# Kernel tuning notes

Measured on AMD Instinct MI355X. Metric: run time of the kernel, lower is better.

## Reference

```python
import jax, jax.numpy as jnp
import numpy as np

N_USERS = 100000
EMBED_DIM = 128
N_EDGES = 640000


def setup_inputs() -> dict:
    key = jax.random.key(0)
    k1, k2, k3, k4, k5, k6 = jax.random.split(key, 6)
    # Xavier-normal-ish scale for embedding table
    emb = jax.random.normal(k1, (N_USERS, EMBED_DIM), dtype=jnp.float32) * 0.02
    s = 1.0 / np.sqrt(EMBED_DIM)
    W_l = jax.random.normal(k2, (EMBED_DIM, EMBED_DIM), dtype=jnp.float32) * s
    b_l = jax.random.normal(k3, (EMBED_DIM,), dtype=jnp.float32) * 0.01
    W_r = jax.random.normal(k4, (EMBED_DIM, EMBED_DIM), dtype=jnp.float32) * s
    src = jax.random.randint(k5, (N_EDGES,), 0, N_USERS, dtype=jnp.int64)
    dst = jax.random.randint(k6, (N_EDGES,), 0, N_USERS, dtype=jnp.int64)
    return {"emb": emb, "W_l": W_l, "b_l": b_l, "W_r": W_r, "src": src, "dst": dst}


def reference(emb, W_l, b_l, W_r, src, dst):
    # GraphSAGE (mean aggr) over the full user embedding table.
    # messages gathered from source nodes: [E, D]
    msgs = emb[src]
    agg = jax.ops.segment_sum(msgs, dst, num_segments=N_USERS)  # [N, D]
    deg = jax.ops.segment_sum(jnp.ones((dst.shape[0],), dtype=emb.dtype), dst,
                              num_segments=N_USERS)
    agg = agg / jnp.maximum(deg, 1.0)[:, None]  # mean over neighbors
    # out = lin_l(mean neighbors) + lin_r(self); bias on lin_l only (PyG SAGEConv)
    out = agg @ W_l.T + b_l + emb @ W_r.T
    # dropout (p=0) and batchnorm (is_norm=False) are identity here
    return out
```

## Files before the change

### kernel.cpp

```cpp
#include <hip/hip_runtime.h>
#include <hip/hip_bf16.h>

#define N_USERS   100000
#define EMBED_DIM 128
#define N_EDGES   640000
#define ZERO_ROW  N_USERS

typedef __bf16 bf16x8 __attribute__((ext_vector_type(8)));
typedef float  f32x4  __attribute__((ext_vector_type(4)));

#define OFF_COUNTS 25600256
#define OFF_TOTAL  26000256
#define OFF_START  26000384
#define OFF_CURSOR 26400384
#define OFF_PERM   26800384
#define OFF_WLSW   30560384
#define OFF_WRSW   30593152
#define OFF_AGGB   30625920

__device__ __forceinline__ unsigned short f2bf_rne(float f) {
    union { float f; unsigned u; } c; c.f = f;
    unsigned u = c.u + 0x7fffu + ((c.u >> 16) & 1u);
    return (unsigned short)(u >> 16);
}
__device__ __forceinline__ float bf2f_lo(unsigned u) {
    union { float f; unsigned u; } c; c.u = u << 16;
    return c.f;
}
__device__ __forceinline__ float bf2f_hi(unsigned u) {
    union { float f; unsigned u; } c; c.u = u & 0xffff0000u;
    return c.f;
}

__global__ __launch_bounds__(256) void k_init(const float* __restrict__ emb,
                                              const float* __restrict__ Wl,
                                              const float* __restrict__ Wr,
                                              const int* __restrict__ dst,
                                              unsigned short* __restrict__ embb,
                                              int* __restrict__ counts,
                                              unsigned short* __restrict__ wlsw,
                                              unsigned short* __restrict__ wrsw) {
    int i = blockIdx.x * 256 + threadIdx.x;
    if (i < 2048) {
        int li = i & 63;
        int kt = (i >> 6) & 3;
        int jt = i >> 8;
        int row  = jt * 16 + (li & 15);
        int colb = kt * 32 + ((li >> 4) << 3);
        const float4* pl = (const float4*)(Wl + row * 128 + colb);
        const float4* pr = (const float4*)(Wr + row * 128 + colb);
        float4 l0 = pl[0], l1 = pl[1];
        float4 r0 = pr[0], r1 = pr[1];
        int o = i * 8;
        wlsw[o+0] = f2bf_rne(l0.x); wlsw[o+1] = f2bf_rne(l0.y);
        wlsw[o+2] = f2bf_rne(l0.z); wlsw[o+3] = f2bf_rne(l0.w);
        wlsw[o+4] = f2bf_rne(l1.x); wlsw[o+5] = f2bf_rne(l1.y);
        wlsw[o+6] = f2bf_rne(l1.z); wlsw[o+7] = f2bf_rne(l1.w);
        wrsw[o+0] = f2bf_rne(r0.x); wrsw[o+1] = f2bf_rne(r0.y);
        wrsw[o+2] = f2bf_rne(r0.z); wrsw[o+3] = f2bf_rne(r0.w);
        wrsw[o+4] = f2bf_rne(r1.x); wrsw[o+5] = f2bf_rne(r1.y);
        wrsw[o+6] = f2bf_rne(r1.z); wrsw[o+7] = f2bf_rne(r1.w);
    }
    if (i < 16) {
        int4 z = {0, 0, 0, 0};
        ((int4*)(embb + (size_t)ZERO_ROW * EMBED_DIM))[i] = z;
    }
    float4 a = ((const float4*)emb)[i * 2 + 0];
    float4 b = ((const float4*)emb)[i * 2 + 1];
    int4 p;
    p.x = (int)f2bf_rne(a.x) | ((int)f2bf_rne(a.y) << 16);
    p.y = (int)f2bf_rne(a.z) | ((int)f2bf_rne(a.w) << 16);
    p.z = (int)f2bf_rne(b.x) | ((int)f2bf_rne(b.y) << 16);
    p.w = (int)f2bf_rne(b.z) | ((int)f2bf_rne(b.w) << 16);
    ((int4*)embb)[i] = p;
    if (i < N_EDGES) atomicAdd(&counts[dst[i]], 1);
}

__global__ __launch_bounds__(256) void k_alloc(const int* __restrict__ counts,
                                               int* __restrict__ start,
                                               int* __restrict__ cursor,
                                               int* __restrict__ total,
                                               int* __restrict__ perm) {
    int i    = blockIdx.x * 256 + threadIdx.x;
    int lane = threadIdx.x & 63;
    int wv   = threadIdx.x >> 6;
    int4 c4 = {0, 0, 0, 0};
    if (i < 25000) c4 = ((const int4*)counts)[i];
    int4 p4;
    p4.x = (c4.x + 3) & ~3;
    p4.y = (c4.y + 3) & ~3;
    p4.z = (c4.z + 3) & ~3;
    p4.w = (c4.w + 3) & ~3;
    int csum = p4.x + p4.y + p4.z + p4.w;
    int pre = csum;
#pragma unroll
    for (int d = 1; d < 64; d <<= 1) {
        int v = __shfl_up(pre, d);
        if (lane >= d) pre += v;
    }
    __shared__ int swv[4];
    __shared__ int sgbase;
    if (lane == 63) swv[wv] = pre;
    __syncthreads();
    if (threadIdx.x == 0)
        sgbase = atomicAdd(total, swv[0] + swv[1] + swv[2] + swv[3]);
    __syncthreads();
    int waveoff = 0;
    for (int w = 0; w < wv; w++) waveoff += swv[w];
    int base = sgbase + waveoff + (pre - csum);
    if (i < 25000) {
        int4 s;
        s.x = base;
        s.y = s.x + p4.x;
        s.z = s.y + p4.y;
        s.w = s.z + p4.z;
        ((int4*)start)[i]  = s;
        ((int4*)cursor)[i] = s;
        for (int k = c4.x; k < p4.x; k++) perm[s.x + k] = ZERO_ROW;
        for (int k = c4.y; k < p4.y; k++) perm[s.y + k] = ZERO_ROW;
        for (int k = c4.z; k < p4.z; k++) perm[s.z + k] = ZERO_ROW;
        for (int k = c4.w; k < p4.w; k++) perm[s.w + k] = ZERO_ROW;
    }
}

__global__ __launch_bounds__(256) void k_perm(const int* __restrict__ src,
                                              const int* __restrict__ dst,
                                              int* __restrict__ cursor,
                                              int* __restrict__ perm) {
    int e = blockIdx.x * 256 + threadIdx.x;
    if (e < N_EDGES) {
        int pos = atomicAdd(&cursor[dst[e]], 1);
        perm[pos] = src[e];
    }
}

__global__ __launch_bounds__(256) void k_aggregate(const unsigned short* __restrict__ embb,
                                                   const int* __restrict__ start,
                                                   const int* __restrict__ counts,
                                                   const int* __restrict__ perm,
                                                   unsigned short* __restrict__ aggb) {
    int gw   = (blockIdx.x * 256 + threadIdx.x) >> 6;
    int lane = threadIdx.x & 63;
    int nA = gw * 2;
    int nB = nA + 1;
    int sA = start[nA], cntA = counts[nA];
    int sB = start[nB], cntB = counts[nB];
    int ga = (cntA + 3) >> 2;
    int gb = (cntB + 3) >> 2;
    int gmin = ga < gb ? ga : gb;
    float2 accA = {0.f, 0.f}, accB = {0.f, 0.f};
    const unsigned short* ep = embb;
    int off = lane * 2;

    int t = 0;
    for (; t < gmin; t++) {
        int4 ia = ((const int4*)(perm + sA))[t];
        int4 ib = ((const int4*)(perm + sB))[t];
        unsigned a0 = *(const unsigned*)(ep + (size_t)ia.x * EMBED_DIM + off);
        unsigned a1 = *(const unsigned*)(ep + (size_t)ia.y * EMBED_DIM + off);
        unsigned a2 = *(const unsigned*)(ep + (size_t)ia.z * EMBED_DIM + off);
        unsigned a3 = *(const unsigned*)(ep + (size_t)ia.w * EMBED_DIM + off);
        unsigned b0 = *(const unsigned*)(ep + (size_t)ib.x * EMBED_DIM + off);
        unsigned b1 = *(const unsigned*)(ep + (size_t)ib.y * EMBED_DIM + off);
        unsigned b2 = *(const unsigned*)(ep + (size_t)ib.z * EMBED_DIM + off);
        unsigned b3 = *(const unsigned*)(ep + (size_t)ib.w * EMBED_DIM + off);
        accA.x += (bf2f_lo(a0) + bf2f_lo(a1)) + (bf2f_lo(a2) + bf2f_lo(a3));
        accA.y += (bf2f_hi(a0) + bf2f_hi(a1)) + (bf2f_hi(a2) + bf2f_hi(a3));
        accB.x += (bf2f_lo(b0) + bf2f_lo(b1)) + (bf2f_lo(b2) + bf2f_lo(b3));
        accB.y += (bf2f_hi(b0) + bf2f_hi(b1)) + (bf2f_hi(b2) + bf2f_hi(b3));
    }
    for (int ta = t; ta < ga; ta++) {
        int4 ia = ((const int4*)(perm + sA))[ta];
        unsigned a0 = *(const unsigned*)(ep + (size_t)ia.x * EMBED_DIM + off);
        unsigned a1 = *(const unsigned*)(ep + (size_t)ia.y * EMBED_DIM + off);
        unsigned a2 = *(const unsigned*)(ep + (size_t)ia.z * EMBED_DIM + off);
        unsigned a3 = *(const unsigned*)(ep + (size_t)ia.w * EMBED_DIM + off);
        accA.x += (bf2f_lo(a0) + bf2f_lo(a1)) + (bf2f_lo(a2) + bf2f_lo(a3));
        accA.y += (bf2f_hi(a0) + bf2f_hi(a1)) + (bf2f_hi(a2) + bf2f_hi(a3));
    }
    for (int tb = t; tb < gb; tb++) {
        int4 ib = ((const int4*)(perm + sB))[tb];
        unsigned b0 = *(const unsigned*)(ep + (size_t)ib.x * EMBED_DIM + off);
        unsigned b1 = *(const unsigned*)(ep + (size_t)ib.y * EMBED_DIM + off);
        unsigned b2 = *(const unsigned*)(ep + (size_t)ib.z * EMBED_DIM + off);
        unsigned b3 = *(const unsigned*)(ep + (size_t)ib.w * EMBED_DIM + off);
        accB.x += (bf2f_lo(b0) + bf2f_lo(b1)) + (bf2f_lo(b2) + bf2f_lo(b3));
        accB.y += (bf2f_hi(b0) + bf2f_hi(b1)) + (bf2f_hi(b2) + bf2f_hi(b3));
    }
    float invA = (cntA > 0) ? 1.0f / (float)cntA : 0.0f;
    float invB = (cntB > 0) ? 1.0f / (float)cntB : 0.0f;
    unsigned oA = (unsigned)f2bf_rne(accA.x * invA) | ((unsigned)f2bf_rne(accA.y * invA) << 16);
    unsigned oB = (unsigned)f2bf_rne(accB.x * invB) | ((unsigned)f2bf_rne(accB.y * invB) << 16);
    *(unsigned*)(aggb + (size_t)nA * EMBED_DIM + off) = oA;
    *(unsigned*)(aggb + (size_t)nB * EMBED_DIM + off) = oB;
}

#define LDS_S 136
__global__ __launch_bounds__(256) void k_matmul(const unsigned short* __restrict__ aggb,
                                                const unsigned short* __restrict__ wlsw,
                                                const unsigned short* __restrict__ wrsw,
                                                const unsigned short* __restrict__ embb,
                                                const float* __restrict__ bl,
                                                float* __restrict__ out) {
    __shared__ unsigned short sa[32 * LDS_S];
    __shared__ unsigned short se[32 * LDS_S];
    int tid  = threadIdx.x;
    int wave = tid >> 6;
    int lane = tid & 63;
    int quad = lane >> 4;
    int m    = lane & 15;
    int jt0  = wave * 2;
    int node0 = blockIdx.x * 32;

    bf16x8 wl[2][4], wr[2][4];
#pragma unroll
    for (int jj = 0; jj < 2; jj++) {
#pragma unroll
        for (int kt = 0; kt < 4; kt++) {
            size_t o = (size_t)((((jt0 + jj) * 4 + kt) * 64 + lane)) * 8;
            wl[jj][kt] = *(const bf16x8*)((const __bf16*)wlsw + o);
            wr[jj][kt] = *(const bf16x8*)((const __bf16*)wrsw + o);
        }
    }
    float bias[2];
    bias[0] = bl[(jt0 + 0) * 16 + m];
    bias[1] = bl[(jt0 + 1) * 16 + m];

    const int4* aslab = (const int4*)(aggb + (size_t)node0 * EMBED_DIM);
    const int4* eslab = (const int4*)(embb + (size_t)node0 * EMBED_DIM);
#pragma unroll
    for (int p = 0; p < 2; p++) {
        int g   = p * 256 + tid;
        int row = g >> 4;
        int c   = g & 15;
        int4 va = aslab[g];
        int4 ve = eslab[g];
        *(int4*)(sa + row * LDS_S + c * 8) = va;
        *(int4*)(se + row * LDS_S + c * 8) = ve;
    }
    __syncthreads();

    bf16x8 af[2][4], ef[2][4];
#pragma unroll
    for (int rt = 0; rt < 2; rt++) {
#pragma unroll
        for (int kt = 0; kt < 4; kt++) {
            int o = (rt * 16 + m) * LDS_S + kt * 32 + quad * 8;
            af[rt][kt] = *(const bf16x8*)(sa + o);
            ef[rt][kt] = *(const bf16x8*)(se + o);
        }
    }

#pragma unroll
    for (int rt = 0; rt < 2; rt++) {
        f32x4 acc[2] = {{0.f,0.f,0.f,0.f}, {0.f,0.f,0.f,0.f}};
#pragma unroll
        for (int kt = 0; kt < 4; kt++) {
#pragma unroll
            for (int jj = 0; jj < 2; jj++) {
                acc[jj] = __builtin_amdgcn_mfma_f32_16x16x32_bf16(af[rt][kt], wl[jj][kt], acc[jj], 0, 0, 0);
                acc[jj] = __builtin_amdgcn_mfma_f32_16x16x32_bf16(ef[rt][kt], wr[jj][kt], acc[jj], 0, 0, 0);
            }
        }
#pragma unroll
        for (int jj = 0; jj < 2; jj++) {
#pragma unroll
            for (int r = 0; r < 4; r++) {
                int orow = node0 + rt * 16 + quad * 4 + r;
                out[(size_t)orow * EMBED_DIM + (jt0 + jj) * 16 + m] = acc[jj][r] + bias[jj];
            }
        }
    }
}

extern "C" void kernel_launch(void* const* d_in, const int* in_sizes, int n_in,
                              void* d_out, int out_size, void* d_ws, size_t ws_size,
                              hipStream_t stream) {
    const float* emb = (const float*)d_in[0];
    const float* Wl  = (const float*)d_in[1];
    const float* bl  = (const float*)d_in[2];
    const float* Wr  = (const float*)d_in[3];
    const int*   src = (const int*)d_in[4];
    const int*   dst = (const int*)d_in[5];
    float* out = (float*)d_out;

    char* ws = (char*)d_ws;
    unsigned short* embb   = (unsigned short*)ws;
    int*            counts = (int*)(ws + OFF_COUNTS);
    int*            total  = (int*)(ws + OFF_TOTAL);
    int*            start  = (int*)(ws + OFF_START);
    int*            cursor = (int*)(ws + OFF_CURSOR);
    int*            perm   = (int*)(ws + OFF_PERM);
    unsigned short* wlsw   = (unsigned short*)(ws + OFF_WLSW);
    unsigned short* wrsw   = (unsigned short*)(ws + OFF_WRSW);
    unsigned short* aggb   = (unsigned short*)(ws + OFF_AGGB);

    hipMemsetAsync(ws + OFF_COUNTS, 0, (OFF_TOTAL - OFF_COUNTS) + 4, stream);

    k_init<<<6250, 256, 0, stream>>>(emb, Wl, Wr, dst, embb, counts, wlsw, wrsw);
    k_alloc<<<98, 256, 0, stream>>>(counts, start, cursor, total, perm);
    k_perm<<<2500, 256, 0, stream>>>(src, dst, cursor, perm);
    k_aggregate<<<12500, 256, 0, stream>>>(embb, start, counts, perm, aggb);
    k_matmul<<<3125, 256, 0, stream>>>(aggb, wlsw, wrsw, embb, bl, out);
}
```

Before: 214.2 us.

## Fuse neighbor aggregation into the MFMA matmul kernel via shared memory

Merges the separate aggregation and matmul kernels into one kernel. Each block gathers and averages neighbor rows for its 32 nodes and writes the bf16 means straight into LDS instead of a global agg buffer. This removes a kernel launch and the write and re-read of the 25 MB aggregate, and it prefetches the self-embedding slab ahead of the gather. The cost is fewer, heavier blocks: each wave now handles 8 nodes serially, which may expose gather latency. A launch-bounds hint of 4 blocks per CU and a smaller fragment register footprint are added to keep occupancy up.

```diff
diff --git a/kernel.cpp b/kernel.cpp
--- a/kernel.cpp
+++ b/kernel.cpp
@@ -16,7 +16,6 @@
 #define OFF_PERM   26800384
 #define OFF_WLSW   30560384
 #define OFF_WRSW   30593152
-#define OFF_AGGB   30625920
 
 __device__ __forceinline__ unsigned short f2bf_rne(float f) {
     union { float f; unsigned u; } c; c.f = f;
@@ -134,74 +133,15 @@
     }
 }
 
-__global__ __launch_bounds__(256) void k_aggregate(const unsigned short* __restrict__ embb,
-                                                   const int* __restrict__ start,
-                                                   const int* __restrict__ counts,
-                                                   const int* __restrict__ perm,
-                                                   unsigned short* __restrict__ aggb) {
-    int gw   = (blockIdx.x * 256 + threadIdx.x) >> 6;
-    int lane = threadIdx.x & 63;
-    int nA = gw * 2;
-    int nB = nA + 1;
-    int sA = start[nA], cntA = counts[nA];
-    int sB = start[nB], cntB = counts[nB];
-    int ga = (cntA + 3) >> 2;
-    int gb = (cntB + 3) >> 2;
-    int gmin = ga < gb ? ga : gb;
-    float2 accA = {0.f, 0.f}, accB = {0.f, 0.f};
-    const unsigned short* ep = embb;
-    int off = lane * 2;
-
-    int t = 0;
-    for (; t < gmin; t++) {
-        int4 ia = ((const int4*)(perm + sA))[t];
-        int4 ib = ((const int4*)(perm + sB))[t];
-        unsigned a0 = *(const unsigned*)(ep + (size_t)ia.x * EMBED_DIM + off);
-        unsigned a1 = *(const unsigned*)(ep + (size_t)ia.y * EMBED_DIM + off);
-        unsigned a2 = *(const unsigned*)(ep + (size_t)ia.z * EMBED_DIM + off);
-        unsigned a3 = *(const unsigned*)(ep + (size_t)ia.w * EMBED_DIM + off);
-        unsigned b0 = *(const unsigned*)(ep + (size_t)ib.x * EMBED_DIM + off);
-        unsigned b1 = *(const unsigned*)(ep + (size_t)ib.y * EMBED_DIM + off);
-        unsigned b2 = *(const unsigned*)(ep + (size_t)ib.z * EMBED_DIM + off);
-        unsigned b3 = *(const unsigned*)(ep + (size_t)ib.w * EMBED_DIM + off);
-        accA.x += (bf2f_lo(a0) + bf2f_lo(a1)) + (bf2f_lo(a2) + bf2f_lo(a3));
-        accA.y += (bf2f_hi(a0) + bf2f_hi(a1)) + (bf2f_hi(a2) + bf2f_hi(a3));
-        accB.x += (bf2f_lo(b0) + bf2f_lo(b1)) + (bf2f_lo(b2) + bf2f_lo(b3));
-        accB.y += (bf2f_hi(b0) + bf2f_hi(b1)) + (bf2f_hi(b2) + bf2f_hi(b3));
-    }
-    for (int ta = t; ta < ga; ta++) {
-        int4 ia = ((const int4*)(perm + sA))[ta];
-        unsigned a0 = *(const unsigned*)(ep + (size_t)ia.x * EMBED_DIM + off);
-        unsigned a1 = *(const unsigned*)(ep + (size_t)ia.y * EMBED_DIM + off);
-        unsigned a2 = *(const unsigned*)(ep + (size_t)ia.z * EMBED_DIM + off);
-        unsigned a3 = *(const unsigned*)(ep + (size_t)ia.w * EMBED_DIM + off);
-        accA.x += (bf2f_lo(a0) + bf2f_lo(a1)) + (bf2f_lo(a2) + bf2f_lo(a3));
-        accA.y += (bf2f_hi(a0) + bf2f_hi(a1)) + (bf2f_hi(a2) + bf2f_hi(a3));
-    }
-    for (int tb = t; tb < gb; tb++) {
-        int4 ib = ((const int4*)(perm + sB))[tb];
-        unsigned b0 = *(const unsigned*)(ep + (size_t)ib.x * EMBED_DIM + off);
-        unsigned b1 = *(const unsigned*)(ep + (size_t)ib.y * EMBED_DIM + off);
-        unsigned b2 = *(const unsigned*)(ep + (size_t)ib.z * EMBED_DIM + off);
-        unsigned b3 = *(const unsigned*)(ep + (size_t)ib.w * EMBED_DIM + off);
-        accB.x += (bf2f_lo(b0) + bf2f_lo(b1)) + (bf2f_lo(b2) + bf2f_lo(b3));
-        accB.y += (bf2f_hi(b0) + bf2f_hi(b1)) + (bf2f_hi(b2) + bf2f_hi(b3));
-    }
-    float invA = (cntA > 0) ? 1.0f / (float)cntA : 0.0f;
-    float invB = (cntB > 0) ? 1.0f / (float)cntB : 0.0f;
-    unsigned oA = (unsigned)f2bf_rne(accA.x * invA) | ((unsigned)f2bf_rne(accA.y * invA) << 16);
-    unsigned oB = (unsigned)f2bf_rne(accB.x * invB) | ((unsigned)f2bf_rne(accB.y * invB) << 16);
-    *(unsigned*)(aggb + (size_t)nA * EMBED_DIM + off) = oA;
-    *(unsigned*)(aggb + (size_t)nB * EMBED_DIM + off) = oB;
-}
-
 #define LDS_S 136
-__global__ __launch_bounds__(256) void k_matmul(const unsigned short* __restrict__ aggb,
-                                                const unsigned short* __restrict__ wlsw,
-                                                const unsigned short* __restrict__ wrsw,
-                                                const unsigned short* __restrict__ embb,
-                                                const float* __restrict__ bl,
-                                                float* __restrict__ out) {
+__global__ __launch_bounds__(256, 4) void k_fused(const unsigned short* __restrict__ embb,
+                                                  const int* __restrict__ start,
+                                                  const int* __restrict__ counts,
+                                                  const int* __restrict__ perm,
+                                                  const unsigned short* __restrict__ wlsw,
+                                                  const unsigned short* __restrict__ wrsw,
+                                                  const float* __restrict__ bl,
+                                                  float* __restrict__ out) {
     __shared__ unsigned short sa[32 * LDS_S];
     __shared__ unsigned short se[32 * LDS_S];
     int tid  = threadIdx.x;
@@ -209,9 +149,77 @@
     int lane = tid & 63;
     int quad = lane >> 4;
     int m    = lane & 15;
-    int jt0  = wave * 2;
     int node0 = blockIdx.x * 32;
 
+    const int4* eslab = (const int4*)(embb + (size_t)node0 * EMBED_DIM);
+    int4 ve0 = eslab[tid];
+    int4 ve1 = eslab[256 + tid];
+
+    const unsigned short* ep = embb;
+    int off = lane * 2;
+#pragma unroll
+    for (int p = 0; p < 4; p++) {
+        int nA = node0 + wave * 8 + p * 2;
+        int nB = nA + 1;
+        int sA = start[nA], cntA = counts[nA];
+        int sB = start[nB], cntB = counts[nB];
+        int ga = (cntA + 3) >> 2;
+        int gb = (cntB + 3) >> 2;
+        int gmin = ga < gb ? ga : gb;
+        float2 accA = {0.f, 0.f}, accB = {0.f, 0.f};
+        int t = 0;
+#pragma unroll 2
+        for (; t < gmin; t++) {
+            int4 ia = ((const int4*)(perm + sA))[t];
+            int4 ib = ((const int4*)(perm + sB))[t];
+            unsigned a0 = *(const unsigned*)(ep + (size_t)ia.x * EMBED_DIM + off);
+            unsigned a1 = *(const unsigned*)(ep + (size_t)ia.y * EMBED_DIM + off);
+            unsigned a2 = *(const unsigned*)(ep + (size_t)ia.z * EMBED_DIM + off);
+            unsigned a3 = *(const unsigned*)(ep + (size_t)ia.w * EMBED_DIM + off);
+            unsigned b0 = *(const unsigned*)(ep + (size_t)ib.x * EMBED_DIM + off);
+            unsigned b1 = *(const unsigned*)(ep + (size_t)ib.y * EMBED_DIM + off);
+            unsigned b2 = *(const unsigned*)(ep + (size_t)ib.z * EMBED_DIM + off);
+            unsigned b3 = *(const unsigned*)(ep + (size_t)ib.w * EMBED_DIM + off);
+            accA.x += (bf2f_lo(a0) + bf2f_lo(a1)) + (bf2f_lo(a2) + bf2f_lo(a3));
+            accA.y += (bf2f_hi(a0) + bf2f_hi(a1)) + (bf2f_hi(a2) + bf2f_hi(a3));
+            accB.x += (bf2f_lo(b0) + bf2f_lo(b1)) + (bf2f_lo(b2) + bf2f_lo(b3));
+            accB.y += (bf2f_hi(b0) + bf2f_hi(b1)) + (bf2f_hi(b2) + bf2f_hi(b3));
+        }
+        for (int ta = t; ta < ga; ta++) {
+            int4 ia = ((const int4*)(perm + sA))[ta];
+            unsigned a0 = *(const unsigned*)(ep + (size_t)ia.x * EMBED_DIM + off);
+            unsigned a1 = *(const unsigned*)(ep + (size_t)ia.y * EMBED_DIM + off);
+            unsigned a2 = *(const unsigned*)(ep + (size_t)ia.z * EMBED_DIM + off);
+            unsigned a3 = *(const unsigned*)(ep + (size_t)ia.w * EMBED_DIM + off);
+            accA.x += (bf2f_lo(a0) + bf2f_lo(a1)) + (bf2f_lo(a2) + bf2f_lo(a3));
+            accA.y += (bf2f_hi(a0) + bf2f_hi(a1)) + (bf2f_hi(a2) + bf2f_hi(a3));
+        }
+        for (int tb = t; tb < gb; tb++) {
+            int4 ib = ((const int4*)(perm + sB))[tb];
+            unsigned b0 = *(const unsigned*)(ep + (size_t)ib.x * EMBED_DIM + off);
+            unsigned b1 = *(const unsigned*)(ep + (size_t)ib.y * EMBED_DIM + off);
+            unsigned b2 = *(const unsigned*)(ep + (size_t)ib.z * EMBED_DIM + off);
+            unsigned b3 = *(const unsigned*)(ep + (size_t)ib.w * EMBED_DIM + off);
+            accB.x += (bf2f_lo(b0) + bf2f_lo(b1)) + (bf2f_lo(b2) + bf2f_lo(b3));
+            accB.y += (bf2f_hi(b0) + bf2f_hi(b1)) + (bf2f_hi(b2) + bf2f_hi(b3));
+        }
+        float invA = (cntA > 0) ? 1.0f / (float)cntA : 0.0f;
+        float invB = (cntB > 0) ? 1.0f / (float)cntB : 0.0f;
+        unsigned oA = (unsigned)f2bf_rne(accA.x * invA) | ((unsigned)f2bf_rne(accA.y * invA) << 16);
+        unsigned oB = (unsigned)f2bf_rne(accB.x * invB) | ((unsigned)f2bf_rne(accB.y * invB) << 16);
+        int nlA = wave * 8 + p * 2;
+        *(unsigned*)(sa + nlA * LDS_S + off)       = oA;
+        *(unsigned*)(sa + (nlA + 1) * LDS_S + off) = oB;
+    }
+
+    {
+        int g = tid, row = g >> 4, c = g & 15;
+        *(int4*)(se + row * LDS_S + c * 8) = ve0;
+        g = 256 + tid; row = g >> 4; c = g & 15;
+        *(int4*)(se + row * LDS_S + c * 8) = ve1;
+    }
+
+    int jt0 = wave * 2;
     bf16x8 wl[2][4], wr[2][4];
 #pragma unroll
     for (int jj = 0; jj < 2; jj++) {
@@ -226,40 +234,24 @@
     bias[0] = bl[(jt0 + 0) * 16 + m];
     bias[1] = bl[(jt0 + 1) * 16 + m];
 
-    const int4* aslab = (const int4*)(aggb + (size_t)node0 * EMBED_DIM);
-    const int4* eslab = (const int4*)(embb + (size_t)node0 * EMBED_DIM);
-#pragma unroll
-    for (int p = 0; p < 2; p++) {
-        int g   = p * 256 + tid;
-        int row = g >> 4;
-        int c   = g & 15;
-        int4 va = aslab[g];
-        int4 ve = eslab[g];
-        *(int4*)(sa + row * LDS_S + c * 8) = va;
-        *(int4*)(se + row * LDS_S + c * 8) = ve;
-    }
     __syncthreads();
 
-    bf16x8 af[2][4], ef[2][4];
 #pragma unroll
     for (int rt = 0; rt < 2; rt++) {
+        bf16x8 af[4], ef[4];
 #pragma unroll
         for (int kt = 0; kt < 4; kt++) {
             int o = (rt * 16 + m) * LDS_S + kt * 32 + quad * 8;
-            af[rt][kt] = *(const bf16x8*)(sa + o);
-            ef[rt][kt] = *(const bf16x8*)(se + o);
-        }
-    }
-
-#pragma unroll
-    for (int rt = 0; rt < 2; rt++) {
+            af[kt] = *(const bf16x8*)(sa + o);
+            ef[kt] = *(const bf16x8*)(se + o);
+        }
         f32x4 acc[2] = {{0.f,0.f,0.f,0.f}, {0.f,0.f,0.f,0.f}};
 #pragma unroll
         for (int kt = 0; kt < 4; kt++) {
 #pragma unroll
             for (int jj = 0; jj < 2; jj++) {
-                acc[jj] = __builtin_amdgcn_mfma_f32_16x16x32_bf16(af[rt][kt], wl[jj][kt], acc[jj], 0, 0, 0);
-                acc[jj] = __builtin_amdgcn_mfma_f32_16x16x32_bf16(ef[rt][kt], wr[jj][kt], acc[jj], 0, 0, 0);
+                acc[jj] = __builtin_amdgcn_mfma_f32_16x16x32_bf16(af[kt], wl[jj][kt], acc[jj], 0, 0, 0);
+                acc[jj] = __builtin_amdgcn_mfma_f32_16x16x32_bf16(ef[kt], wr[jj][kt], acc[jj], 0, 0, 0);
             }
         }
 #pragma unroll
@@ -293,13 +285,11 @@
     int*            perm   = (int*)(ws + OFF_PERM);
     unsigned short* wlsw   = (unsigned short*)(ws + OFF_WLSW);
     unsigned short* wrsw   = (unsigned short*)(ws + OFF_WRSW);
-    unsigned short* aggb   = (unsigned short*)(ws + OFF_AGGB);
 
     hipMemsetAsync(ws + OFF_COUNTS, 0, (OFF_TOTAL - OFF_COUNTS) + 4, stream);
 
     k_init<<<6250, 256, 0, stream>>>(emb, Wl, Wr, dst, embb, counts, wlsw, wrsw);
     k_alloc<<<98, 256, 0, stream>>>(counts, start, cursor, total, perm);
     k_perm<<<2500, 256, 0, stream>>>(src, dst, cursor, perm);
-    k_aggregate<<<12500, 256, 0, stream>>>(embb, start, counts, perm, aggb);
-    k_matmul<<<3125, 256, 0, stream>>>(aggb, wlsw, wrsw, embb, bl, out);
-}
+    k_fused<<<3125, 256, 0, stream>>>(embb, start, counts, perm, wlsw, wrsw, bl, out);
+}
```

After: 214.3 us. Within noise of the previous version (+0.1%).
